# Optimization experiments

Measured on AMD Instinct MI355X. Metric: run time of the kernel, lower is better.

## Reference

```python
import jax, jax.numpy as jnp
import numpy as np

# Camera model constants (expected-value camera: gain multiply + baseline offset)
GAIN = 2.0
BASELINE = 100.0

B, E = 32, 64          # frames, emitters per frame
H = W = 128            # image size
R = 13                 # PSF ROI (patch) size
D = 32                 # number of z slices in the spline table


def setup_inputs() -> dict:
    key = jax.random.key(0)
    k1, k2, k3, k4 = jax.random.split(key, 4)
    # subpixel emitter positions: x in [0,W), y in [0,H), z in voxel units [0, D-1)
    u = jax.random.uniform(k1, (B, E, 3), dtype=jnp.float32)
    xyz = u * jnp.array([W, H, D - 1], dtype=jnp.float32)
    n_photons = 1000.0 + 4000.0 * jax.random.uniform(k2, (B, E), dtype=jnp.float32)
    bg = 10.0 + 90.0 * jax.random.uniform(k3, (B, H, W), dtype=jnp.float32)
    # cubic-spline coefficient table: [z_slice, roi_y, roi_x, 4(dz),4(dy),4(dx)]
    coeff = 0.01 * jax.random.normal(k4, (D, R, R, 4, 4, 4), dtype=jnp.float32)
    return {"xyz": xyz, "n_photons": n_photons, "bg": bg, "coeff": coeff}


def reference(xyz, n_photons, bg, coeff):
    Bb, Hh, Ww = bg.shape
    Dd, Rr = coeff.shape[0], coeff.shape[1]
    half = Rr // 2
    pow4 = jnp.arange(4)

    def render_one(pos, nph):
        x, y, z = pos[0], pos[1], pos[2]
        xf, yf = jnp.floor(x), jnp.floor(y)
        dx, dy = x - xf, y - yf
        zc = jnp.clip(z, 0.0, Dd - 1.0 - 1e-6)
        zf = jnp.floor(zc)
        zi = zf.astype(jnp.int32)
        dz = zc - zf
        px = dx ** pow4  # [4]
        py = dy ** pow4
        pz = dz ** pow4
        c = coeff[zi]  # [R,R,4,4,4] gather of this emitter's z-slice
        patch = jnp.einsum('yxabc,a,b,c->yx', c, pz, py, px) * nph  # [R,R]
        r0 = yf.astype(jnp.int32) - half
        c0 = xf.astype(jnp.int32) - half
        rows = r0 + jnp.arange(Rr)
        cols = c0 + jnp.arange(Rr)
        img = jnp.zeros((Hh, Ww), patch.dtype)
        # irregular scatter-add of the PSF patch; OOB (incl. negative) dropped
        return img.at[rows[:, None], cols[None, :]].add(patch, mode='drop')

    imgs = jax.vmap(jax.vmap(render_one))(xyz, n_photons)  # [B,E,H,W]
    y = imgs + bg[:, None]          # add background per frame
    return y * GAIN + BASELINE      # camera gain
```

## Files before the change

### kernel.cpp

```cpp
#include <hip/hip_runtime.h>

constexpr int   B = 32, E = 64, H = 128, W = 128, R = 13, D = 32;
constexpr float GAIN = 2.0f, BASELINE = 100.0f;
constexpr int   HALF = R / 2;
constexpr int   PLANE = H * W;
constexpr int   PLANE4 = PLANE / 4;

__device__ __forceinline__ float pw(float v, int p) {
    float r = 1.0f;
    if (p >= 1) r = v;
    if (p >= 2) r *= v;
    if (p >= 3) r *= v;
    return r;
}

__global__ __launch_bounds__(256)
void stream_bg_kernel(const float* __restrict__ bg,
                      float* __restrict__ out)
{
    const int tid = threadIdx.x;
    const long long base4 = (long long)blockIdx.x * 1024;
    #pragma unroll
    for (int j = 0; j < 4; ++j) {
        const long long idx4 = base4 + j * 256 + tid;
        const int within4 = (int)(idx4 & (PLANE4 - 1));
        const int b       = (int)(idx4 >> 18);
        const float4 v = *(const float4*)(bg + ((size_t)b << 14) + ((size_t)within4 << 2));
        float4 o;
        o.x = v.x * GAIN + BASELINE;
        o.y = v.y * GAIN + BASELINE;
        o.z = v.z * GAIN + BASELINE;
        o.w = v.w * GAIN + BASELINE;
        *(float4*)(out + (idx4 << 2)) = o;
    }
}

__global__ __launch_bounds__(256)
void patch_kernel(const float* __restrict__ xyz,
                  const float* __restrict__ n_photons,
                  const float* __restrict__ bg,
                  const float* __restrict__ coeff,
                  float* __restrict__ out)
{
    const int be  = blockIdx.x;
    const int b   = be >> 6;
    const int tid = threadIdx.x;

    __shared__ float s_w[64];

    const float x = xyz[be * 3 + 0];
    const float y = xyz[be * 3 + 1];
    const float z = xyz[be * 3 + 2];
    const float nph = n_photons[be];

    const float xf = floorf(x), yf = floorf(y);
    const float dx = x - xf,   dy = y - yf;
    float zc = fminf(fmaxf(z, 0.0f), (float)(D - 1) - 1e-6f);
    const float zf = floorf(zc);
    const int   zi = (int)zf;
    const float dz = zc - zf;

    const int r0 = (int)yf - HALF;
    const int c0 = (int)xf - HALF;

    if (tid < 64) {
        const int a  = tid >> 4;
        const int bb = (tid >> 2) & 3;
        const int c  = tid & 3;
        s_w[tid] = pw(dz, a) * pw(dy, bb) * pw(dx, c);
    }
    __syncthreads();

    if (tid < R * R) {
        const int pr = tid / R;
        const int pc = tid - pr * R;

        const float* cp = coeff + (((size_t)zi * R + pr) * R + pc) * 64;
        float acc = 0.0f;
        #pragma unroll
        for (int k = 0; k < 64; k += 4) {
            const float4 cc = *(const float4*)(cp + k);
            acc += cc.x * s_w[k + 0];
            acc += cc.y * s_w[k + 1];
            acc += cc.z * s_w[k + 2];
            acc += cc.w * s_w[k + 3];
        }
        const float patch = acc * nph;

        int row = r0 + pr;  if (row < 0) row += H;
        int col = c0 + pc;  if (col < 0) col += W;
        if (row < H && col < W) {
            const size_t ppix = ((size_t)(row << 7)) + col;
            const float  bgv  = bg[((size_t)b << 14) + ppix];
            out[((size_t)be << 14) + ppix] = (bgv + patch) * GAIN + BASELINE;
        }
    }
}

extern "C" void kernel_launch(void* const* d_in, const int* in_sizes, int n_in,
                              void* d_out, int out_size, void* d_ws, size_t ws_size,
                              hipStream_t stream) {
    const float* xyz       = (const float*)d_in[0];
    const float* n_photons = (const float*)d_in[1];
    const float* bg        = (const float*)d_in[2];
    const float* coeff     = (const float*)d_in[3];
    float* out = (float*)d_out;

    stream_bg_kernel<<<dim3(8192), dim3(256), 0, stream>>>(bg, out);
    patch_kernel<<<dim3(B * E), dim3(256), 0, stream>>>(xyz, n_photons, bg, coeff, out);
}
```

Baseline: 161.7 us.

## Fuse background streaming and patch scatter into one kernel with nontemporal stores

Replaces the two-kernel scheme (stream bg to every output plane, then overwrite patch pixels) with one kernel. Each block handles a 32-row quarter of one emitter's output plane, builds the patch rows in shared memory, adds them to the background and writes each pixel once with nontemporal vector stores. This removes the second launch and the extra read-modify traffic of the patch pass. In exchange every block recomputes the patch (4x redundant coefficient work) and zeroes a 13x128 shared buffer.

Result: slower. 184.5 us (+14.1%).

```diff
diff --git a/kernel.cpp b/kernel.cpp
--- a/kernel.cpp
+++ b/kernel.cpp
@@ -4,7 +4,8 @@
 constexpr float GAIN = 2.0f, BASELINE = 100.0f;
 constexpr int   HALF = R / 2;
 constexpr int   PLANE = H * W;
-constexpr int   PLANE4 = PLANE / 4;
+
+typedef float v4f __attribute__((ext_vector_type(4)));
 
 __device__ __forceinline__ float pw(float v, int p) {
     float r = 1.0f;
@@ -15,38 +16,21 @@
 }
 
 __global__ __launch_bounds__(256)
-void stream_bg_kernel(const float* __restrict__ bg,
-                      float* __restrict__ out)
+void render_fused_kernel(const float* __restrict__ xyz,
+                         const float* __restrict__ n_photons,
+                         const float* __restrict__ bg,
+                         const float* __restrict__ coeff,
+                         float* __restrict__ out)
 {
-    const int tid = threadIdx.x;
-    const long long base4 = (long long)blockIdx.x * 1024;
-    #pragma unroll
-    for (int j = 0; j < 4; ++j) {
-        const long long idx4 = base4 + j * 256 + tid;
-        const int within4 = (int)(idx4 & (PLANE4 - 1));
-        const int b       = (int)(idx4 >> 18);
-        const float4 v = *(const float4*)(bg + ((size_t)b << 14) + ((size_t)within4 << 2));
-        float4 o;
-        o.x = v.x * GAIN + BASELINE;
-        o.y = v.y * GAIN + BASELINE;
-        o.z = v.z * GAIN + BASELINE;
-        o.w = v.w * GAIN + BASELINE;
-        *(float4*)(out + (idx4 << 2)) = o;
-    }
-}
-
-__global__ __launch_bounds__(256)
-void patch_kernel(const float* __restrict__ xyz,
-                  const float* __restrict__ n_photons,
-                  const float* __restrict__ bg,
-                  const float* __restrict__ coeff,
-                  float* __restrict__ out)
-{
-    const int be  = blockIdx.x;
+    const int blk = blockIdx.x;
+    const int be  = blk >> 2;
+    const int jb  = blk & 3;
     const int b   = be >> 6;
     const int tid = threadIdx.x;
+    const int base_row = jb << 5;
 
     __shared__ float s_w[64];
+    __shared__ float s_row[R * W];
 
     const float x = xyz[be * 3 + 0];
     const float y = xyz[be * 3 + 1];
@@ -63,6 +47,8 @@
     const int r0 = (int)yf - HALF;
     const int c0 = (int)xf - HALF;
 
+    #pragma unroll
+    for (int i = tid; i < R * W; i += 256) s_row[i] = 0.0f;
     if (tid < 64) {
         const int a  = tid >> 4;
         const int bb = (tid >> 2) & 3;
@@ -74,26 +60,44 @@
     if (tid < R * R) {
         const int pr = tid / R;
         const int pc = tid - pr * R;
-
         const float* cp = coeff + (((size_t)zi * R + pr) * R + pc) * 64;
         float acc = 0.0f;
         #pragma unroll
         for (int k = 0; k < 64; k += 4) {
-            const float4 cc = *(const float4*)(cp + k);
+            const v4f cc = *(const v4f*)(cp + k);
             acc += cc.x * s_w[k + 0];
             acc += cc.y * s_w[k + 1];
             acc += cc.z * s_w[k + 2];
             acc += cc.w * s_w[k + 3];
         }
-        const float patch = acc * nph;
+        int col = c0 + pc;
+        if (col < 0) col += W;
+        if (col < W)
+            s_row[pr * W + col] = acc * nph;
+    }
+    __syncthreads();
 
-        int row = r0 + pr;  if (row < 0) row += H;
-        int col = c0 + pc;  if (col < 0) col += W;
-        if (row < H && col < W) {
-            const size_t ppix = ((size_t)(row << 7)) + col;
-            const float  bgv  = bg[((size_t)b << 14) + ppix];
-            out[((size_t)be << 14) + ppix] = (bgv + patch) * GAIN + BASELINE;
+    const float* __restrict__ bgp  = bg  + ((size_t)b  << 14);
+    float*       __restrict__ outp = out + ((size_t)be << 14);
+
+    #pragma unroll
+    for (int j = 0; j < 4; ++j) {
+        const int i   = j * 256 + tid;
+        const int row = base_row + (i >> 5);
+        const int col = (i & 31) << 2;
+        const size_t off = ((size_t)row << 7) + col;
+
+        v4f v = *(const v4f*)(bgp + off);
+
+        int pr = row - r0;
+        if (pr < 0 || pr >= R) pr = row - r0 - 128;
+        if (pr >= 0 && pr < R) {
+            const v4f p = *(const v4f*)(s_row + pr * W + col);
+            v += p;
         }
+
+        v = v * GAIN + BASELINE;
+        __builtin_nontemporal_store(v, (v4f*)(outp + off));
     }
 }
 
@@ -106,6 +110,6 @@
     const float* coeff     = (const float*)d_in[3];
     float* out = (float*)d_out;
 
-    stream_bg_kernel<<<dim3(8192), dim3(256), 0, stream>>>(bg, out);
-    patch_kernel<<<dim3(B * E), dim3(256), 0, stream>>>(xyz, n_photons, bg, coeff, out);
+    render_fused_kernel<<<dim3(B * E * 4), dim3(256), 0, stream>>>(
+        xyz, n_photons, bg, coeff, out);
 }
```
